# Performance work log

Measured on AMD Instinct MI355X. Metric: run time of the kernel, lower is better.

Reference implementation:

```python
import jax, jax.numpy as jnp
import numpy as np

D = 8        # q_ndim (= dof_ndim)
HID = 200    # hidden_size
N = 16384    # batch of states
EPS = 0.1    # qdot regularizer coefficient in L()


def _lagrangian(z, Ws, bs):
    # z: (2D,) = [q, qdot]; angular_dims=() so CosSin is an identity pass-through
    v = z[D:]
    h = z
    for W, b in zip(Ws[:-1], bs[:-1]):
        h = jax.nn.softplus(h @ W + b)   # FCsoftplus blocks
    L = (h @ Ws[-1] + bs[-1])[0]          # final Linear -> scalar (Reshape(-1))
    return L + EPS * jnp.dot(v, v)


def setup_inputs():
    key = jax.random.key(0)
    ks = jax.random.split(key, 5)
    z = jax.random.normal(ks[0], (N, 2 * D), dtype=jnp.float32)
    t = jnp.zeros((), dtype=jnp.float32)

    def lin(k, fi, fo, scale):
        return (jax.random.normal(k, (fi, fo), dtype=jnp.float32)
                * jnp.float32(scale / np.sqrt(fi)))

    W0 = lin(ks[1], 2 * D, HID, 1.0)
    W1 = lin(ks[2], HID, HID, 1.0)
    W2 = lin(ks[3], HID, HID, 1.0)
    W3 = lin(ks[4], HID, 1, 0.01)  # small head keeps mass matrix M well conditioned
    b0 = jnp.zeros((HID,), jnp.float32)  # zero_bias init per FCsoftplus/Linear
    b1 = jnp.zeros((HID,), jnp.float32)
    b2 = jnp.zeros((HID,), jnp.float32)
    b3 = jnp.zeros((1,), jnp.float32)
    return dict(t=t, z=z, W0=W0, b0=b0, W1=W1, b1=b1, W2=W2, b2=b2, W3=W3, b3=b3)


def reference(t, z, W0, b0, W1, b1, W2, b2, W3, b3):
    # Euler-Lagrange dynamics (LagrangianDynamics):
    #   M a = dL/dq - (d2L/dq dv) v,  M = d2L/dv2;  dz/dt = [v, a]
    Ws = (W0, W1, W2, W3)
    bs = (b0, b1, b2, b3)
    Lfn = lambda zz: _lagrangian(zz, Ws, bs)

    def dyn_single(zi):
        g = jax.grad(Lfn)(zi)              # (2D,)  = [dL/dq, dL/dv]
        H = jax.jacfwd(jax.grad(Lfn))(zi)  # (2D,2D) Hessian of L wrt z
        v = zi[D:]
        M = H[D:, D:]                      # d(dL/dv)/dv  -> mass matrix
        C = H[D:, :D]                      # d(dL/dv)/dq
        F = g[:D] - C @ v
        a = jnp.linalg.solve(M, F)
        return jnp.concatenate([v, a])     # (2D,)

    return jax.vmap(dyn_single)(z)         # (N, 2D)
```

## Files before the change

kernel.cpp:

```cpp
#include <hip/hip_runtime.h>
#include <math.h>

#define DD 8
#define ZD 16
#define HID 200
#define EPSL 0.1f
#define BS 16
#define NTHREADS 1024
#define NKC 7
#define NMT 13
#define XSTR 216
#define CSTR 216
#define WSTR 208
#define HSTR 20
#define NT4 4

#define KSC 1024.0f
#define SSC 64.0f
#define INV_K (1.0f/1024.0f)
#define INV_KS (1.0f/65536.0f)

typedef _Float16 half8 __attribute__((ext_vector_type(8)));
typedef _Float16 half4v __attribute__((ext_vector_type(4)));
typedef _Float16 half2v __attribute__((ext_vector_type(2)));
typedef float float4v __attribute__((ext_vector_type(4)));

#define S4 (NKC*NMT*64*8)
#define OFF_W1T 0
#define OFF_W2T (S4)
#define OFF_W1  (2*S4)
#define OFF_W2  (3*S4)
#define OFF_W0T (4*S4)
#define OFF_W0  (4*S4 + NMT*64*8)
#define WS_HALFS (4*S4 + NMT*64*8 + NKC*64*8)

#define CFSZ  (16*CSTR)
#define O_XT  0
#define O_XB  (128*XSTR + 8)
#define O_CF  (O_XB + 128*XSTR)
#define O_BSH (O_CF + 5*CFSZ)
#define O_W0T (O_BSH + 4*WSTR)
#define O_XZ  (O_W0T + 8*WSTR + 24)
#define O_GSH (O_XZ + 16*40)
#define O_HR  (O_GSH + 256)
#define SMEM_HALFS (O_HR + 128*HSTR*2)

__global__ void prep(const float* __restrict__ W0, const float* __restrict__ W1,
                     const float* __restrict__ W2, _Float16* __restrict__ ws)
{
    int idx = blockIdx.x * 256 + threadIdx.x;
    if (idx >= WS_HALFS) return;
    float v = 0.f;
    if (idx < 4*S4) {
        int arr = idx / S4, e = idx % S4;
        int kc = e / (NMT*64*8); int r = e % (NMT*64*8);
        int mt = r / (64*8); r %= 64*8;
        int lane = r / 8, j = r % 8;
        int m = mt*16 + (lane & 15);
        int k = kc*32 + (lane >> 4)*8 + j;
        if (m < HID && k < HID) {
            if      (arr == 0) v = W1[k*HID + m];
            else if (arr == 1) v = W2[k*HID + m];
            else if (arr == 2) v = W1[m*HID + k];
            else               v = W2[m*HID + k];
        }
    } else if (idx < OFF_W0) {
        int e = idx - OFF_W0T;
        int mt = e / (64*8); int r = e % (64*8);
        int lane = r / 8, j = r % 8;
        int m = mt*16 + (lane & 15);
        int k = (lane >> 4)*8 + j;
        if (m < HID && k < ZD) v = W0[k*HID + m];
    } else {
        int e = idx - OFF_W0;
        int kc = e / (64*8); int r = e % (64*8);
        int lane = r / 8, j = r % 8;
        int m = (lane & 15);
        int k = kc*32 + (lane >> 4)*8 + j;
        if (k < HID) v = W0[m*HID + k];
    }
    ws[idx] = (_Float16)v;
}

__device__ __forceinline__ half4v pk4(float4v a) {
    half2v lo = __builtin_bit_cast(half2v, __builtin_amdgcn_cvt_pkrtz(a.x, a.y));
    half2v hi = __builtin_bit_cast(half2v, __builtin_amdgcn_cvt_pkrtz(a.z, a.w));
    return __builtin_shufflevector(lo, hi, 0, 1, 2, 3);
}
__device__ __forceinline__ void sig_sp(float x, float& sp, float& sg) {
    float e = __expf(-fabsf(x));
    float r = 1.0f / (1.0f + e);
    sg = (x >= 0.f) ? r : (1.0f - r);
    sp = fmaxf(x, 0.f) + __logf(1.f + e);
}

template<int NTILES>
__device__ __forceinline__ void run_mv(const half8* __restrict__ Asw,
                                       const _Float16* __restrict__ Xsrc,
                                       int mt0, int mtc, int lane,
                                       float4v acc[2][NTILES])
{
    const int lm = lane & 15, q = lane >> 4;
#pragma unroll
    for (int m = 0; m < 2; ++m)
#pragma unroll
        for (int n = 0; n < NTILES; ++n)
            acc[m][n] = (float4v){0.f, 0.f, 0.f, 0.f};
    for (int kc = 0; kc < NKC; ++kc) {
        half8 a[2];
#pragma unroll
        for (int m = 0; m < 2; ++m)
            if (m < mtc) a[m] = Asw[(kc*NMT + mt0 + m)*64 + lane];
        half8 x[NTILES];
#pragma unroll
        for (int n = 0; n < NTILES; ++n)
            x[n] = *(const half8*)(Xsrc + (n*16 + lm)*XSTR + kc*32 + q*8);
#pragma unroll
        for (int m = 0; m < 2; ++m)
            if (m < mtc)
#pragma unroll
                for (int n = 0; n < NTILES; ++n)
                    acc[m][n] = __builtin_amdgcn_mfma_f32_16x16x32_f16(a[m], x[n], acc[m][n], 0, 0, 0);
    }
}

__global__ void __launch_bounds__(NTHREADS, 4)
lnn_main(const float* __restrict__ z,
         const float* __restrict__ W0, const float* __restrict__ b0,
         const float* __restrict__ b1, const float* __restrict__ b2,
         const float* __restrict__ W3,
         const _Float16* __restrict__ ws,
         float* __restrict__ out)
{
    __shared__ alignas(16) _Float16 smem[SMEM_HALFS];
    _Float16* const Xt  = smem + O_XT;
    _Float16* const Xb  = smem + O_XB;
    _Float16* const Cf  = smem + O_CF;
    _Float16* const bsh = smem + O_BSH;
    _Float16* const w0t = smem + O_W0T;
    _Float16* const Xz  = smem + O_XZ;
    float*    const gsh = (float*)(smem + O_GSH);
    float*    const Hr  = (float*)(smem + O_HR);
    _Float16* const FB  = smem + O_HR;

    const int tid  = threadIdx.x;
    const int wave = tid >> 6;
    const int lane = tid & 63;
    const int lm   = lane & 15;
    const int q    = lane >> 4;
    const int s0   = blockIdx.x * BS;

    const int twm  = wave >> 1;
    const int twn  = wave & 1;
    const int mt0t = (twm < 5) ? twm*2 : (twm + 5);
    const int mtct = (twm < 5) ? 2 : 1;

    const half8* W1Tsw = (const half8*)(ws + OFF_W1T);
    const half8* W2Tsw = (const half8*)(ws + OFF_W2T);
    const half8* W1sw  = (const half8*)(ws + OFF_W1);
    const half8* W2sw  = (const half8*)(ws + OFF_W2);
    const half8* W0Tsw = (const half8*)(ws + OFF_W0T);
    const half8* W0sw  = (const half8*)(ws + OFF_W0);

    if (tid < 256) {
        int s = tid >> 4, k = tid & 15;
        Xz[s*40 + k]      = (_Float16)z[(s0 + s)*ZD + k];
        Xz[s*40 + 16 + k] = (_Float16)0.f;
    }
    for (int idx = tid; idx < 128*16; idx += NTHREADS) {
        int r = idx >> 4, c = 200 + (idx & 15);
        Xt[r*XSTR + c] = (_Float16)0.f;
        Xb[r*XSTR + c] = (_Float16)0.f;
    }
    for (int idx = tid; idx < 16*16; idx += NTHREADS) {
        int r = idx >> 4, c = 200 + (idx & 15);
        FB[r*XSTR + c] = (_Float16)0.f;
    }
    if (tid < 8) {
        Xt[128*XSTR + tid] = (_Float16)0.f;
        FB[16*XSTR + tid]  = (_Float16)0.f;
    }
    for (int idx = tid; idx < 5*16*8; idx += NTHREADS) {
        int j = idx >> 7, r = (idx >> 3) & 15, c = 208 + (idx & 7);
        Cf[j*CFSZ + r*CSTR + c] = (_Float16)0.f;
    }
    for (int idx = tid; idx < 4*WSTR; idx += NTHREADS) {
        int l = idx / WSTR, u = idx % WSTR;
        float v = 0.f;
        if (u < HID) {
            if      (l == 0) v = b0[u];
            else if (l == 1) v = b1[u];
            else if (l == 2) v = b2[u];
            else             v = KSC * W3[u];
        }
        bsh[idx] = (_Float16)v;
    }
    for (int idx = tid; idx < 8*WSTR + 24; idx += NTHREADS) {
        int t = idx / WSTR, u = idx % WSTR;
        w0t[idx] = (_Float16)((t < 8 && u < HID) ? SSC * W0[(DD + t)*HID + u] : 0.f);
    }
    __syncthreads();

    float4v acc1[2][1];
    float4v acc4[2][NT4];
    const int ubf = wave*16 + q*4;

    if (wave < NMT) {
        acc1[0][0] = (float4v){0.f,0.f,0.f,0.f};
        half8 xz = *(const half8*)(Xz + lm*40 + q*8);
        half8 aw = W0Tsw[wave*64 + lane];
        acc1[0][0] = __builtin_amdgcn_mfma_f32_16x16x32_f16(aw, xz, acc1[0][0], 0, 0, 0);
        half4v bb = *(const half4v*)(&bsh[0*WSTR + ubf]);
        float h[4], p[4];
#pragma unroll
        for (int r = 0; r < 4; ++r) {
            float av = acc1[0][0][r] + (float)bb[r];
            sig_sp(av, h[r], p[r]);
        }
        *(half4v*)(&FB[lm*XSTR + ubf])          = pk4((float4v){h[0],h[1],h[2],h[3]});
        *(half4v*)(&Cf[0*CFSZ + lm*CSTR + ubf]) = pk4((float4v){p[0],p[1],p[2],p[3]});
    }
    __syncthreads();

    if (wave < NMT) run_mv<1>(W1Tsw, FB, wave, 1, lane, acc1);
    __syncthreads();
    if (wave < NMT) {
        half4v bb = *(const half4v*)(&bsh[1*WSTR + ubf]);
        float h[4], p[4];
#pragma unroll
        for (int r = 0; r < 4; ++r) {
            float av = acc1[0][0][r] + (float)bb[r];
            sig_sp(av, h[r], p[r]);
        }
        *(half4v*)(&FB[lm*XSTR + ubf])          = pk4((float4v){h[0],h[1],h[2],h[3]});
        *(half4v*)(&Cf[1*CFSZ + lm*CSTR + ubf]) = pk4((float4v){p[0],p[1],p[2],p[3]});
    }
    __syncthreads();

    {
#pragma unroll
        for (int m = 0; m < 2; ++m)
#pragma unroll
            for (int n = 0; n < NT4; ++n)
                acc4[m][n] = (float4v){0.f, 0.f, 0.f, 0.f};
        for (int kc = 0; kc < NKC; ++kc) {
            half8 a[2];
#pragma unroll
            for (int m = 0; m < 2; ++m)
                if (m < mtct) a[m] = W1Tsw[(kc*NMT + mt0t + m)*64 + lane];
            half8 p0 = *(const half8*)(Cf + 0*CFSZ + lm*CSTR + kc*32 + q*8);
            half8 x[NT4];
#pragma unroll
            for (int n = 0; n < NT4; ++n) {
                half8 w0 = *(const half8*)(w0t + (twn*NT4 + n)*WSTR + kc*32 + q*8);
                x[n] = p0 * w0;
            }
#pragma unroll
            for (int m = 0; m < 2; ++m)
                if (m < mtct)
#pragma unroll
                    for (int n = 0; n < NT4; ++n)
                        acc4[m][n] = __builtin_amdgcn_mfma_f32_16x16x32_f16(a[m], x[n], acc4[m][n], 0, 0, 0);
        }
        if (wave < NMT) run_mv<1>(W2Tsw, FB, wave, 1, lane, acc1);
    }
    __syncthreads();
#pragma unroll
    for (int m = 0; m < 2; ++m)
        if (m < mtct) {
            const int ub = (mt0t + m)*16 + q*4;
            half4v p1 = *(const half4v*)(&Cf[1*CFSZ + lm*CSTR + ub]);
#pragma unroll
            for (int n = 0; n < NT4; ++n) {
                int row = (twn*NT4 + n)*16 + lm;
                *(half4v*)(&Xt[row*XSTR + ub]) = pk4(acc4[m][n]) * p1;
            }
        }
    if (wave < NMT) {
        half4v bb = *(const half4v*)(&bsh[2*WSTR + ubf]);
        half4v w3 = *(const half4v*)(&bsh[3*WSTR + ubf]);
        float d2[4], c2[4];
#pragma unroll
        for (int r = 0; r < 4; ++r) {
            float av = acc1[0][0][r] + (float)bb[r];
            float e = __expf(-fabsf(av));
            float rr = 1.f / (1.f + e);
            float sg = (av >= 0.f) ? rr : (1.f - rr);
            float wk = (float)w3[r];
            d2[r] = wk * sg;
            c2[r] = wk * sg * (1.f - sg);
        }
        *(half4v*)(&FB[lm*XSTR + ubf])          = pk4((float4v){d2[0],d2[1],d2[2],d2[3]});
        *(half4v*)(&Cf[2*CFSZ + lm*CSTR + ubf]) = pk4((float4v){c2[0],c2[1],c2[2],c2[3]});
    }
    __syncthreads();

    run_mv<NT4>(W2Tsw, Xt + twn*64*XSTR, mt0t, mtct, lane, acc4);
    if (wave < NMT) run_mv<1>(W2sw, FB, wave, 1, lane, acc1);
    __syncthreads();
#pragma unroll
    for (int m = 0; m < 2; ++m)
        if (m < mtct) {
            const int ub = (mt0t + m)*16 + q*4;
            half4v c2 = *(const half4v*)(&Cf[2*CFSZ + lm*CSTR + ub]);
#pragma unroll
            for (int n = 0; n < NT4; ++n) {
                int row = (twn*NT4 + n)*16 + lm;
                *(half4v*)(&Xb[row*XSTR + ub]) = pk4(acc4[m][n]) * c2;
            }
        }
    if (wave < NMT) {
        half4v p1 = *(const half4v*)(&Cf[1*CFSZ + lm*CSTR + ubf]);
        half4v u1 = pk4(acc1[0][0]);
        half4v one = {(_Float16)1.f,(_Float16)1.f,(_Float16)1.f,(_Float16)1.f};
        *(half4v*)(&FB[lm*XSTR + ubf])          = u1 * p1;
        *(half4v*)(&Cf[3*CFSZ + lm*CSTR + ubf]) = u1 * (one - p1);
    }
    __syncthreads();

    run_mv<NT4>(W2sw, Xb + twn*64*XSTR, mt0t, mtct, lane, acc4);
    if (wave < NMT) run_mv<1>(W1sw, FB, wave, 1, lane, acc1);
    __syncthreads();
#pragma unroll
    for (int m = 0; m < 2; ++m)
        if (m < mtct) {
            const int ub = (mt0t + m)*16 + q*4;
            half4v p1 = *(const half4v*)(&Cf[1*CFSZ + lm*CSTR + ub]);
            half4v c3 = *(const half4v*)(&Cf[3*CFSZ + lm*CSTR + ub]);
#pragma unroll
            for (int n = 0; n < NT4; ++n) {
                int row = (twn*NT4 + n)*16 + lm;
                half4v th1 = *(const half4v*)(&Xt[row*XSTR + ub]);
                *(half4v*)(&Xb[row*XSTR + ub]) = pk4(acc4[m][n]) * p1 + c3 * th1;
            }
        }
    if (wave < NMT) {
        half4v p0 = *(const half4v*)(&Cf[0*CFSZ + lm*CSTR + ubf]);
        half4v u0 = pk4(acc1[0][0]);
        half4v one = {(_Float16)1.f,(_Float16)1.f,(_Float16)1.f,(_Float16)1.f};
        half4v d0 = u0 * p0;
        *(half4v*)(&FB[lm*XSTR + ubf])          = d0;
        *(half4v*)(&Cf[4*CFSZ + lm*CSTR + ubf]) = d0 * (one - p0);
    }
    __syncthreads();

    run_mv<NT4>(W1sw, Xb + twn*64*XSTR, mt0t, mtct, lane, acc4);
    if (wave == 13) {
        float4v g = (float4v){0.f,0.f,0.f,0.f};
        for (int kc = 0; kc < NKC; ++kc) {
            half8 a = W0sw[kc*64 + lane];
            half8 x = *(const half8*)(FB + lm*XSTR + kc*32 + q*8);
            g = __builtin_amdgcn_mfma_f32_16x16x32_f16(a, x, g, 0, 0, 0);
        }
        if (q < 2) {
            float4v gv;
            gv.x = g.x*INV_K; gv.y = g.y*INV_K; gv.z = g.z*INV_K; gv.w = g.w*INV_K;
            *(float4v*)(&gsh[lm*8 + q*4]) = gv;
        }
    }
#pragma unroll
    for (int m = 0; m < 2; ++m)
        if (m < mtct) {
            const int ub = (mt0t + m)*16 + q*4;
            half4v p0 = *(const half4v*)(&Cf[0*CFSZ + lm*CSTR + ub]);
            half4v c4 = *(const half4v*)(&Cf[4*CFSZ + lm*CSTR + ub]);
#pragma unroll
            for (int n = 0; n < NT4; ++n) {
                int row = (twn*NT4 + n)*16 + lm;
                half4v w0 = *(const half4v*)(&w0t[(twn*NT4 + n)*WSTR + ub]);
                *(half4v*)(&Xt[row*XSTR + ub]) = pk4(acc4[m][n]) * p0 + c4 * w0;
            }
        }
    __syncthreads();

    if (wave < 8) {
        float4v hacc = (float4v){0.f,0.f,0.f,0.f};
        for (int kc = 0; kc < NKC; ++kc) {
            half8 a = W0sw[kc*64 + lane];
            half8 x = *(const half8*)(Xt + (wave*16 + lm)*XSTR + kc*32 + q*8);
            hacc = __builtin_amdgcn_mfma_f32_16x16x32_f16(a, x, hacc, 0, 0, 0);
        }
        int row = wave*16 + lm;
        float4v hv;
        hv.x = hacc.x*INV_KS; hv.y = hacc.y*INV_KS;
        hv.z = hacc.z*INV_KS; hv.w = hacc.w*INV_KS;
        *(float4v*)(&Hr[row*HSTR + q*4]) = hv;
    }
    __syncthreads();

    if (tid < BS) {
        const int s = tid;
        float M[DD][DD], F[DD], v[DD], a[DD];
#pragma unroll
        for (int c = 0; c < DD; ++c) v[c] = z[(s0 + s)*ZD + DD + c];
#pragma unroll
        for (int r = 0; r < DD; ++r) {
            float f = gsh[s*8 + r];
#pragma unroll
            for (int c = 0; c < DD; ++c) {
                M[r][c] = Hr[(r*16 + s)*HSTR + DD + c] + ((r == c) ? 2.f*EPSL : 0.f);
                f -= Hr[(r*16 + s)*HSTR + c] * v[c];
            }
            F[r] = f;
        }
#pragma unroll
        for (int col = 0; col < DD; ++col) {
            const float inv = 1.f / M[col][col];
#pragma unroll
            for (int r = col + 1; r < DD; ++r) {
                const float fac = M[r][col] * inv;
#pragma unroll
                for (int c = col + 1; c < DD; ++c) M[r][c] -= fac * M[col][c];
                F[r] -= fac * F[col];
            }
        }
#pragma unroll
        for (int r = DD - 1; r >= 0; --r) {
            float ssum = F[r];
#pragma unroll
            for (int c = r + 1; c < DD; ++c) ssum -= M[r][c] * a[c];
            a[r] = ssum / M[r][r];
        }
        float* op = out + (size_t)(s0 + s)*ZD;
#pragma unroll
        for (int c = 0; c < DD; ++c) { op[c] = v[c]; op[DD + c] = a[c]; }
    }
}

extern "C" void kernel_launch(void* const* d_in, const int* in_sizes, int n_in,
                              void* d_out, int out_size, void* d_ws, size_t ws_size,
                              hipStream_t stream)
{
    const float* z  = (const float*)d_in[1];
    const float* W0 = (const float*)d_in[2];
    const float* b0 = (const float*)d_in[3];
    const float* W1 = (const float*)d_in[4];
    const float* b1 = (const float*)d_in[5];
    const float* W2 = (const float*)d_in[6];
    const float* b2 = (const float*)d_in[7];
    const float* W3 = (const float*)d_in[8];
    float* out = (float*)d_out;
    _Float16* ws = (_Float16*)d_ws;

    const int n = in_sizes[1] / (2*DD);

    prep<<<dim3((WS_HALFS + 255)/256), dim3(256), 0, stream>>>(W0, W1, W2, ws);
    lnn_main<<<dim3(n / BS), dim3(NTHREADS), 0, stream>>>(
        z, W0, b0, b1, b2, W3, ws, out);
}
```

Before: 156.6 us.

## Skew forward/backward vector chain against tangent GEMMs and prefetch weight fragments

Reschedules the per-sample gradient chain (forward layers and backward vector products) so that it runs one stage ahead on waves 3-15 and overlaps with the tangent GEMM stages. It uses double-buffered FB scratch areas so that consecutive stages do not collide. The change removes several block-wide barriers. It also prefetches the first A-fragment of each weight matrix into registers before the barrier and fully unrolls the k-loops. The cost is extra register pressure and more complex shared-memory aliasing; the Hr region now overlaps the FB and gsh buffers.

After: 153.0 us. 1.02x faster.

```diff
diff --git a/kernel.cpp b/kernel.cpp
--- a/kernel.cpp
+++ b/kernel.cpp
@@ -11,6 +11,8 @@
 #define NMT 13
 #define XSTR 216
 #define CSTR 216
+#define FBSTR 216
+#define BSTR 208
 #define WSTR 208
 #define HSTR 20
 #define NT4 4
@@ -35,15 +37,17 @@
 #define WS_HALFS (4*S4 + NMT*64*8 + NKC*64*8)
 
 #define CFSZ  (16*CSTR)
+#define FBSZ  (16*FBSTR + 8)
 #define O_XT  0
 #define O_XB  (128*XSTR + 8)
-#define O_CF  (O_XB + 128*XSTR)
-#define O_BSH (O_CF + 5*CFSZ)
-#define O_W0T (O_BSH + 4*WSTR)
-#define O_XZ  (O_W0T + 8*WSTR + 24)
-#define O_GSH (O_XZ + 16*40)
-#define O_HR  (O_GSH + 256)
-#define SMEM_HALFS (O_HR + 128*HSTR*2)
+#define O_CF  (2*(128*XSTR + 8))
+#define O_U   (O_CF + 5*CFSZ)
+#define O_FBA (O_U)
+#define O_FBB (O_U + FBSZ)
+#define O_GS  (O_U + 5120)
+#define O_BSH (O_U + 2*FBSZ)
+#define O_W0T (O_BSH + 3*BSTR)
+#define SMEM_HALFS (O_W0T + 8*WSTR + 24)
 
 __global__ void prep(const float* __restrict__ W0, const float* __restrict__ W1,
                      const float* __restrict__ W2, _Float16* __restrict__ ws)
@@ -94,33 +98,49 @@
     sp = fmaxf(x, 0.f) + __logf(1.f + e);
 }
 
-template<int NTILES>
-__device__ __forceinline__ void run_mv(const half8* __restrict__ Asw,
-                                       const _Float16* __restrict__ Xsrc,
-                                       int mt0, int mtc, int lane,
-                                       float4v acc[2][NTILES])
+__device__ __forceinline__ float4v run_fv(const half8* __restrict__ Asw,
+                                          const _Float16* __restrict__ FBx,
+                                          int fw, int lane, half8 pa)
 {
     const int lm = lane & 15, q = lane >> 4;
+    float4v acc = (float4v){0.f, 0.f, 0.f, 0.f};
+#pragma unroll
+    for (int kc = 0; kc < NKC; ++kc) {
+        half8 a = kc ? Asw[(kc*NMT + fw)*64 + lane] : pa;
+        half8 x = *(const half8*)(FBx + lm*FBSTR + kc*32 + q*8);
+        acc = __builtin_amdgcn_mfma_f32_16x16x32_f16(a, x, acc, 0, 0, 0);
+    }
+    return acc;
+}
+
+template<int NT>
+__device__ __forceinline__ void run_mvp(const half8* __restrict__ Asw,
+                                        const _Float16* __restrict__ Xsrc,
+                                        int mt0, int mtc, int lane,
+                                        float4v acc[2][NT], half8 pa0, half8 pa1)
+{
+    const int lm = lane & 15, q = lane >> 4;
 #pragma unroll
     for (int m = 0; m < 2; ++m)
 #pragma unroll
-        for (int n = 0; n < NTILES; ++n)
+        for (int n = 0; n < NT; ++n)
             acc[m][n] = (float4v){0.f, 0.f, 0.f, 0.f};
+#pragma unroll
     for (int kc = 0; kc < NKC; ++kc) {
-        half8 a[2];
-#pragma unroll
-        for (int m = 0; m < 2; ++m)
-            if (m < mtc) a[m] = Asw[(kc*NMT + mt0 + m)*64 + lane];
-        half8 x[NTILES];
-#pragma unroll
-        for (int n = 0; n < NTILES; ++n)
+        half8 a0 = kc ? Asw[(kc*NMT + mt0)*64 + lane] : pa0;
+        half8 a1 = pa1;
+        if (kc && mtc > 1) a1 = Asw[(kc*NMT + mt0 + 1)*64 + lane];
+        half8 x[NT];
+#pragma unroll
+        for (int n = 0; n < NT; ++n)
             x[n] = *(const half8*)(Xsrc + (n*16 + lm)*XSTR + kc*32 + q*8);
 #pragma unroll
-        for (int m = 0; m < 2; ++m)
-            if (m < mtc)
-#pragma unroll
-                for (int n = 0; n < NTILES; ++n)
-                    acc[m][n] = __builtin_amdgcn_mfma_f32_16x16x32_f16(a[m], x[n], acc[m][n], 0, 0, 0);
+        for (int n = 0; n < NT; ++n)
+            acc[0][n] = __builtin_amdgcn_mfma_f32_16x16x32_f16(a0, x[n], acc[0][n], 0, 0, 0);
+        if (mtc > 1)
+#pragma unroll
+            for (int n = 0; n < NT; ++n)
+                acc[1][n] = __builtin_amdgcn_mfma_f32_16x16x32_f16(a1, x[n], acc[1][n], 0, 0, 0);
     }
 }
 
@@ -136,12 +156,12 @@
     _Float16* const Xt  = smem + O_XT;
     _Float16* const Xb  = smem + O_XB;
     _Float16* const Cf  = smem + O_CF;
+    _Float16* const FBa = smem + O_FBA;
+    _Float16* const FBb = smem + O_FBB;
     _Float16* const bsh = smem + O_BSH;
     _Float16* const w0t = smem + O_W0T;
-    _Float16* const Xz  = smem + O_XZ;
-    float*    const gsh = (float*)(smem + O_GSH);
-    float*    const Hr  = (float*)(smem + O_HR);
-    _Float16* const FB  = smem + O_HR;
+    float*    const gsh = (float*)(smem + O_GS);
+    float*    const Hr  = (float*)(smem + O_U);
 
     const int tid  = threadIdx.x;
     const int wave = tid >> 6;
@@ -155,6 +175,10 @@
     const int mt0t = (twm < 5) ? twm*2 : (twm + 5);
     const int mtct = (twm < 5) ? 2 : 1;
 
+    const bool fok = (wave >= 3);
+    const int  fw  = fok ? (wave - 3) : 0;
+    const int  ubf = fw*16 + q*4;
+
     const half8* W1Tsw = (const half8*)(ws + OFF_W1T);
     const half8* W2Tsw = (const half8*)(ws + OFF_W2T);
     const half8* W1sw  = (const half8*)(ws + OFF_W1);
@@ -162,35 +186,38 @@
     const half8* W0Tsw = (const half8*)(ws + OFF_W0T);
     const half8* W0sw  = (const half8*)(ws + OFF_W0);
 
-    if (tid < 256) {
-        int s = tid >> 4, k = tid & 15;
-        Xz[s*40 + k]      = (_Float16)z[(s0 + s)*ZD + k];
-        Xz[s*40 + 16 + k] = (_Float16)0.f;
-    }
+    const half4v one = {(_Float16)1.f,(_Float16)1.f,(_Float16)1.f,(_Float16)1.f};
+
+    float4v acc4[2][NT4];
+    float4v accF;
+    half8 pT0, pT1, pF;
+
     for (int idx = tid; idx < 128*16; idx += NTHREADS) {
         int r = idx >> 4, c = 200 + (idx & 15);
         Xt[r*XSTR + c] = (_Float16)0.f;
         Xb[r*XSTR + c] = (_Float16)0.f;
     }
-    for (int idx = tid; idx < 16*16; idx += NTHREADS) {
-        int r = idx >> 4, c = 200 + (idx & 15);
-        FB[r*XSTR + c] = (_Float16)0.f;
+    for (int idx = tid; idx < 2*16*16; idx += NTHREADS) {
+        int buf = idx >> 8, r = (idx >> 4) & 15, c = 200 + (idx & 15);
+        (buf ? FBb : FBa)[r*FBSTR + c] = (_Float16)0.f;
     }
     if (tid < 8) {
-        Xt[128*XSTR + tid] = (_Float16)0.f;
-        FB[16*XSTR + tid]  = (_Float16)0.f;
+        Xt[128*XSTR + tid]  = (_Float16)0.f;
+        Xb[128*XSTR + tid]  = (_Float16)0.f;
+        FBa[16*FBSTR + tid] = (_Float16)0.f;
+        FBb[16*FBSTR + tid] = (_Float16)0.f;
+        Cf[1*CFSZ + tid]    = (_Float16)0.f;
     }
     for (int idx = tid; idx < 5*16*8; idx += NTHREADS) {
         int j = idx >> 7, r = (idx >> 3) & 15, c = 208 + (idx & 7);
         Cf[j*CFSZ + r*CSTR + c] = (_Float16)0.f;
     }
-    for (int idx = tid; idx < 4*WSTR; idx += NTHREADS) {
-        int l = idx / WSTR, u = idx % WSTR;
+    for (int idx = tid; idx < 3*BSTR; idx += NTHREADS) {
+        int l = idx / BSTR, u = idx % BSTR;
         float v = 0.f;
         if (u < HID) {
-            if      (l == 0) v = b0[u];
-            else if (l == 1) v = b1[u];
-            else if (l == 2) v = b2[u];
+            if      (l == 0) v = b1[u];
+            else if (l == 1) v = b2[u];
             else             v = KSC * W3[u];
         }
         bsh[idx] = (_Float16)v;
@@ -199,42 +226,31 @@
         int t = idx / WSTR, u = idx % WSTR;
         w0t[idx] = (_Float16)((t < 8 && u < HID) ? SSC * W0[(DD + t)*HID + u] : 0.f);
     }
-    __syncthreads();
-
-    float4v acc1[2][1];
-    float4v acc4[2][NT4];
-    const int ubf = wave*16 + q*4;
-
-    if (wave < NMT) {
-        acc1[0][0] = (float4v){0.f,0.f,0.f,0.f};
-        half8 xz = *(const half8*)(Xz + lm*40 + q*8);
-        half8 aw = W0Tsw[wave*64 + lane];
-        acc1[0][0] = __builtin_amdgcn_mfma_f32_16x16x32_f16(aw, xz, acc1[0][0], 0, 0, 0);
-        half4v bb = *(const half4v*)(&bsh[0*WSTR + ubf]);
+    if (fok) {
+        half8 xz;
+#pragma unroll
+        for (int j = 0; j < 8; ++j) xz[j] = (_Float16)0.f;
+        if (q < 2) {
+            const float* zp = z + (size_t)(s0 + lm)*ZD + q*8;
+#pragma unroll
+            for (int j = 0; j < 8; ++j) xz[j] = (_Float16)zp[j];
+        }
+        float4v a0v = (float4v){0.f,0.f,0.f,0.f};
+        half8 aw = W0Tsw[fw*64 + lane];
+        a0v = __builtin_amdgcn_mfma_f32_16x16x32_f16(aw, xz, a0v, 0, 0, 0);
         float h[4], p[4];
 #pragma unroll
         for (int r = 0; r < 4; ++r) {
-            float av = acc1[0][0][r] + (float)bb[r];
+            float bb = (ubf < HID) ? b0[ubf + r] : 0.f;
+            float av = a0v[r] + bb;
             sig_sp(av, h[r], p[r]);
         }
-        *(half4v*)(&FB[lm*XSTR + ubf])          = pk4((float4v){h[0],h[1],h[2],h[3]});
+        *(half4v*)(&FBa[lm*FBSTR + ubf])        = pk4((float4v){h[0],h[1],h[2],h[3]});
         *(half4v*)(&Cf[0*CFSZ + lm*CSTR + ubf]) = pk4((float4v){p[0],p[1],p[2],p[3]});
     }
-    __syncthreads();
-
-    if (wave < NMT) run_mv<1>(W1Tsw, FB, wave, 1, lane, acc1);
-    __syncthreads();
-    if (wave < NMT) {
-        half4v bb = *(const half4v*)(&bsh[1*WSTR + ubf]);
-        float h[4], p[4];
-#pragma unroll
-        for (int r = 0; r < 4; ++r) {
-            float av = acc1[0][0][r] + (float)bb[r];
-            sig_sp(av, h[r], p[r]);
-        }
-        *(half4v*)(&FB[lm*XSTR + ubf])          = pk4((float4v){h[0],h[1],h[2],h[3]});
-        *(half4v*)(&Cf[1*CFSZ + lm*CSTR + ubf]) = pk4((float4v){p[0],p[1],p[2],p[3]});
-    }
+    pT0 = W1Tsw[mt0t*64 + lane];
+    pT1 = W1Tsw[(mt0t + mtct - 1)*64 + lane];
+    pF  = W1Tsw[fw*64 + lane];
     __syncthreads();
 
     {
@@ -243,11 +259,11 @@
 #pragma unroll
             for (int n = 0; n < NT4; ++n)
                 acc4[m][n] = (float4v){0.f, 0.f, 0.f, 0.f};
+#pragma unroll
         for (int kc = 0; kc < NKC; ++kc) {
-            half8 a[2];
-#pragma unroll
-            for (int m = 0; m < 2; ++m)
-                if (m < mtct) a[m] = W1Tsw[(kc*NMT + mt0t + m)*64 + lane];
+            half8 a0 = kc ? W1Tsw[(kc*NMT + mt0t)*64 + lane] : pT0;
+            half8 a1 = pT1;
+            if (kc && mtct > 1) a1 = W1Tsw[(kc*NMT + mt0t + 1)*64 + lane];
             half8 p0 = *(const half8*)(Cf + 0*CFSZ + lm*CSTR + kc*32 + q*8);
             half8 x[NT4];
 #pragma unroll
@@ -256,33 +272,37 @@
                 x[n] = p0 * w0;
             }
 #pragma unroll
-            for (int m = 0; m < 2; ++m)
-                if (m < mtct)
-#pragma unroll
-                    for (int n = 0; n < NT4; ++n)
-                        acc4[m][n] = __builtin_amdgcn_mfma_f32_16x16x32_f16(a[m], x[n], acc4[m][n], 0, 0, 0);
-        }
-        if (wave < NMT) run_mv<1>(W2Tsw, FB, wave, 1, lane, acc1);
-    }
-    __syncthreads();
-#pragma unroll
-    for (int m = 0; m < 2; ++m)
-        if (m < mtct) {
-            const int ub = (mt0t + m)*16 + q*4;
-            half4v p1 = *(const half4v*)(&Cf[1*CFSZ + lm*CSTR + ub]);
-#pragma unroll
-            for (int n = 0; n < NT4; ++n) {
-                int row = (twn*NT4 + n)*16 + lm;
-                *(half4v*)(&Xt[row*XSTR + ub]) = pk4(acc4[m][n]) * p1;
-            }
-        }
-    if (wave < NMT) {
-        half4v bb = *(const half4v*)(&bsh[2*WSTR + ubf]);
-        half4v w3 = *(const half4v*)(&bsh[3*WSTR + ubf]);
+            for (int n = 0; n < NT4; ++n)
+                acc4[0][n] = __builtin_amdgcn_mfma_f32_16x16x32_f16(a0, x[n], acc4[0][n], 0, 0, 0);
+            if (mtct > 1)
+#pragma unroll
+                for (int n = 0; n < NT4; ++n)
+                    acc4[1][n] = __builtin_amdgcn_mfma_f32_16x16x32_f16(a1, x[n], acc4[1][n], 0, 0, 0);
+        }
+    }
+    if (fok) {
+        accF = run_fv(W1Tsw, FBa, fw, lane, pF);
+        half4v bb = *(const half4v*)(&bsh[0*BSTR + ubf]);
+        float h[4], p[4];
+#pragma unroll
+        for (int r = 0; r < 4; ++r) {
+            float av = accF[r] + (float)bb[r];
+            sig_sp(av, h[r], p[r]);
+        }
+        *(half4v*)(&FBb[lm*FBSTR + ubf])        = pk4((float4v){h[0],h[1],h[2],h[3]});
+        *(half4v*)(&Cf[1*CFSZ + lm*CSTR + ubf]) = pk4((float4v){p[0],p[1],p[2],p[3]});
+    }
+    pF = W2Tsw[fw*64 + lane];
+    __syncthreads();
+
+    if (fok) {
+        accF = run_fv(W2Tsw, FBb, fw, lane, pF);
+        half4v bb = *(const half4v*)(&bsh[1*BSTR + ubf]);
+        half4v w3 = *(const half4v*)(&bsh[2*BSTR + ubf]);
         float d2[4], c2[4];
 #pragma unroll
         for (int r = 0; r < 4; ++r) {
-            float av = acc1[0][0][r] + (float)bb[r];
+            float av = accF[r] + (float)bb[r];
             float e = __expf(-fabsf(av));
             float rr = 1.f / (1.f + e);
             float sg = (av >= 0.f) ? rr : (1.f - rr);
@@ -290,14 +310,44 @@
             d2[r] = wk * sg;
             c2[r] = wk * sg * (1.f - sg);
         }
-        *(half4v*)(&FB[lm*XSTR + ubf])          = pk4((float4v){d2[0],d2[1],d2[2],d2[3]});
+        *(half4v*)(&FBa[lm*FBSTR + ubf])        = pk4((float4v){d2[0],d2[1],d2[2],d2[3]});
         *(half4v*)(&Cf[2*CFSZ + lm*CSTR + ubf]) = pk4((float4v){c2[0],c2[1],c2[2],c2[3]});
     }
-    __syncthreads();
-
-    run_mv<NT4>(W2Tsw, Xt + twn*64*XSTR, mt0t, mtct, lane, acc4);
-    if (wave < NMT) run_mv<1>(W2sw, FB, wave, 1, lane, acc1);
-    __syncthreads();
+#pragma unroll
+    for (int m = 0; m < 2; ++m)
+        if (m < mtct) {
+            const int ub = (mt0t + m)*16 + q*4;
+            half4v p1 = *(const half4v*)(&Cf[1*CFSZ + lm*CSTR + ub]);
+#pragma unroll
+            for (int n = 0; n < NT4; ++n) {
+                int row = (twn*NT4 + n)*16 + lm;
+                *(half4v*)(&Xt[row*XSTR + ub]) = pk4(acc4[m][n]) * p1;
+            }
+        }
+    pT0 = W2Tsw[mt0t*64 + lane];
+    pT1 = W2Tsw[(mt0t + mtct - 1)*64 + lane];
+    pF  = W2sw[fw*64 + lane];
+    __syncthreads();
+
+    run_mvp<NT4>(W2Tsw, Xt + twn*64*XSTR, mt0t, mtct, lane, acc4, pT0, pT1);
+    if (fok) {
+        accF = run_fv(W2sw, FBa, fw, lane, pF);
+        half4v p1 = *(const half4v*)(&Cf[1*CFSZ + lm*CSTR + ubf]);
+        half4v u1 = pk4(accF);
+        *(half4v*)(&FBb[lm*FBSTR + ubf])        = u1 * p1;
+        *(half4v*)(&Cf[3*CFSZ + lm*CSTR + ubf]) = u1 * (one - p1);
+    }
+    pF = W1sw[fw*64 + lane];
+    __syncthreads();
+
+    if (fok) {
+        accF = run_fv(W1sw, FBb, fw, lane, pF);
+        half4v p0 = *(const half4v*)(&Cf[0*CFSZ + lm*CSTR + ubf]);
+        half4v u0 = pk4(accF);
+        half4v d0 = u0 * p0;
+        *(half4v*)(&FBa[lm*FBSTR + ubf])        = d0;
+        *(half4v*)(&Cf[4*CFSZ + lm*CSTR + ubf]) = d0 * (one - p0);
+    }
 #pragma unroll
     for (int m = 0; m < 2; ++m)
         if (m < mtct) {
@@ -309,18 +359,28 @@
                 *(half4v*)(&Xb[row*XSTR + ub]) = pk4(acc4[m][n]) * c2;
             }
         }
-    if (wave < NMT) {
-        half4v p1 = *(const half4v*)(&Cf[1*CFSZ + lm*CSTR + ubf]);
-        half4v u1 = pk4(acc1[0][0]);
-        half4v one = {(_Float16)1.f,(_Float16)1.f,(_Float16)1.f,(_Float16)1.f};
-        *(half4v*)(&FB[lm*XSTR + ubf])          = u1 * p1;
-        *(half4v*)(&Cf[3*CFSZ + lm*CSTR + ubf]) = u1 * (one - p1);
-    }
-    __syncthreads();
-
-    run_mv<NT4>(W2sw, Xb + twn*64*XSTR, mt0t, mtct, lane, acc4);
-    if (wave < NMT) run_mv<1>(W1sw, FB, wave, 1, lane, acc1);
-    __syncthreads();
+    pT0 = W2sw[mt0t*64 + lane];
+    pT1 = W2sw[(mt0t + mtct - 1)*64 + lane];
+    if (wave == 14) pF = W0sw[lane];
+    __syncthreads();
+
+    run_mvp<NT4>(W2sw, Xb + twn*64*XSTR, mt0t, mtct, lane, acc4, pT0, pT1);
+    if (wave == 14) {
+        float4v g = (float4v){0.f,0.f,0.f,0.f};
+#pragma unroll
+        for (int kc = 0; kc < NKC; ++kc) {
+            half8 a = kc ? W0sw[kc*64 + lane] : pF;
+            half8 x = *(const half8*)(FBa + lm*FBSTR + kc*32 + q*8);
+            g = __builtin_amdgcn_mfma_f32_16x16x32_f16(a, x, g, 0, 0, 0);
+        }
+        if (q < 2) {
+            float4v gv;
+            gv.x = g.x*INV_K; gv.y = g.y*INV_K; gv.z = g.z*INV_K; gv.w = g.w*INV_K;
+            *(float4v*)(&gsh[lm*8 + q*4]) = gv;
+        }
+    }
+    __syncthreads();
+
 #pragma unroll
     for (int m = 0; m < 2; ++m)
         if (m < mtct) {
@@ -334,30 +394,11 @@
                 *(half4v*)(&Xb[row*XSTR + ub]) = pk4(acc4[m][n]) * p1 + c3 * th1;
             }
         }
-    if (wave < NMT) {
-        half4v p0 = *(const half4v*)(&Cf[0*CFSZ + lm*CSTR + ubf]);
-        half4v u0 = pk4(acc1[0][0]);
-        half4v one = {(_Float16)1.f,(_Float16)1.f,(_Float16)1.f,(_Float16)1.f};
-        half4v d0 = u0 * p0;
-        *(half4v*)(&FB[lm*XSTR + ubf])          = d0;
-        *(half4v*)(&Cf[4*CFSZ + lm*CSTR + ubf]) = d0 * (one - p0);
-    }
-    __syncthreads();
-
-    run_mv<NT4>(W1sw, Xb + twn*64*XSTR, mt0t, mtct, lane, acc4);
-    if (wave == 13) {
-        float4v g = (float4v){0.f,0.f,0.f,0.f};
-        for (int kc = 0; kc < NKC; ++kc) {
-            half8 a = W0sw[kc*64 + lane];
-            half8 x = *(const half8*)(FB + lm*XSTR + kc*32 + q*8);
-            g = __builtin_amdgcn_mfma_f32_16x16x32_f16(a, x, g, 0, 0, 0);
-        }
-        if (q < 2) {
-            float4v gv;
-            gv.x = g.x*INV_K; gv.y = g.y*INV_K; gv.z = g.z*INV_K; gv.w = g.w*INV_K;
-            *(float4v*)(&gsh[lm*8 + q*4]) = gv;
-        }
-    }
+    pT0 = W1sw[mt0t*64 + lane];
+    pT1 = W1sw[(mt0t + mtct - 1)*64 + lane];
+    __syncthreads();
+
+    run_mvp<NT4>(W1sw, Xb + twn*64*XSTR, mt0t, mtct, lane, acc4, pT0, pT1);
 #pragma unroll
     for (int m = 0; m < 2; ++m)
         if (m < mtct) {
@@ -371,12 +412,14 @@
                 *(half4v*)(&Xt[row*XSTR + ub]) = pk4(acc4[m][n]) * p0 + c4 * w0;
             }
         }
+    if (wave < 8) pF = W0sw[lane];
     __syncthreads();
 
     if (wave < 8) {
         float4v hacc = (float4v){0.f,0.f,0.f,0.f};
+#pragma unroll
         for (int kc = 0; kc < NKC; ++kc) {
-            half8 a = W0sw[kc*64 + lane];
+            half8 a = kc ? W0sw[kc*64 + lane] : pF;
             half8 x = *(const half8*)(Xt + (wave*16 + lm)*XSTR + kc*32 + q*8);
             hacc = __builtin_amdgcn_mfma_f32_16x16x32_f16(a, x, hacc, 0, 0, 0);
         }
```
